# Performance work log

Measured on AMD Instinct MI355X. Metric: run time of the kernel, lower is better.

The kernel has to match this reference:

```python
import jax, jax.numpy as jnp
import numpy as np

N_NODES = 500_000
N_EDGES = 4_000_000


def setup_inputs() -> dict:
    key = jax.random.key(0)
    k1, k2, k3, k4 = jax.random.split(key, 4)
    x = jax.random.normal(k1, (N_NODES, 3), dtype=jnp.float32)
    edge_index = jax.random.randint(k2, (2, N_EDGES), 0, N_NODES, dtype=jnp.int32)
    # GCNConv(3, 16) and GCNConv(16, 1): weight [in, out], bias [out]
    W1 = jax.random.normal(k3, (3, 16), dtype=jnp.float32) / np.sqrt(3.0)
    b1 = jnp.zeros((16,), dtype=jnp.float32)
    W2 = jax.random.normal(k4, (16, 1), dtype=jnp.float32) / np.sqrt(16.0)
    b2 = jnp.zeros((1,), dtype=jnp.float32)
    return {"x": x, "edge_index": edge_index, "W1": W1, "b1": b1, "W2": W2, "b2": b2}


def gcn_conv(x, edge_index, W, b):
    """PyG GCNConv: add self-loops, symmetric deg^-1/2 normalization,
    linear transform, scatter-add aggregation to target nodes, bias."""
    n = x.shape[0]
    loop = jnp.arange(n, dtype=edge_index.dtype)
    row = jnp.concatenate([edge_index[0], loop])  # source nodes
    col = jnp.concatenate([edge_index[1], loop])  # target nodes
    deg = jax.ops.segment_sum(jnp.ones_like(col, dtype=x.dtype), col, num_segments=n)
    deg_inv_sqrt = jnp.where(deg > 0, jax.lax.rsqrt(jnp.maximum(deg, 1.0)), 0.0)
    norm = deg_inv_sqrt[row] * deg_inv_sqrt[col]  # [E+N]
    h = x @ W  # [N, out]
    msg = h[row] * norm[:, None]  # gather + scale, [E+N, out]
    out = jax.ops.segment_sum(msg, col, num_segments=n)  # scatter-add
    return out + b


def reference(x, edge_index, W1, b1, W2, b2):
    h = jax.nn.relu(gcn_conv(x, edge_index, W1, b1))
    return gcn_conv(h, edge_index, W2, b2)  # [N, 1]
```

## Files before the change

### kernel.cpp

```cpp
#include <hip/hip_runtime.h>
#include <hip/hip_fp16.h>


typedef float vf4 __attribute__((ext_vector_type(4)));

#define NB 512
#define SHIFT 10
#define SLICE 1024
#define CAP 11264
#define P1T 1024
#define P1PER 16
#define P1G 256
#define SENT 0xFFFFFFFFu

__global__ __launch_bounds__(1024) void p1_partition(
        const int* __restrict__ row, const int* __restrict__ col,
        unsigned* __restrict__ gcur, unsigned* __restrict__ buf, int E) {
    __shared__ unsigned hist[NB];
    __shared__ unsigned loff[NB], lcur[NB], gbase[NB];
    __shared__ unsigned stage[P1T * P1PER];
    __shared__ unsigned wsum[16];
    int t = threadIdx.x;
    if (t < NB) hist[t] = 0;
    __syncthreads();
    int per = (E + P1G - 1) / P1G;
    per = (per + 3) & ~3;
    long long base = (long long)blockIdx.x * per;
    long long eend = base + per; if (eend > E) eend = E;
    int nch = (per + 4095) / 4096;
    unsigned ent[P1PER];
    int bkt[P1PER];
#pragma unroll
    for (int ch = 0; ch < 4; ch++) {
        if (ch < nch) {
            long long e = base + (long long)ch * 4096 + 4 * t;
            if (e + 3 < eend) {
                int4 c4 = *(const int4*)(col + e);
                int4 r4 = *(const int4*)(row + e);
                int cs[4] = {c4.x, c4.y, c4.z, c4.w};
                int rs[4] = {r4.x, r4.y, r4.z, r4.w};
#pragma unroll
                for (int u = 0; u < 4; u++) {
                    int j = ch * 4 + u;
                    ent[j] = ((unsigned)rs[u] << SHIFT) | (unsigned)(cs[u] & (SLICE - 1));
                    bkt[j] = cs[u] >> SHIFT;
                    atomicAdd(&hist[bkt[j]], 1u);
                }
            } else {
#pragma unroll
                for (int u = 0; u < 4; u++) {
                    int j = ch * 4 + u;
                    long long ee = e + u;
                    if (ee < eend) {
                        int c = col[ee], r = row[ee];
                        ent[j] = ((unsigned)r << SHIFT) | (unsigned)(c & (SLICE - 1));
                        bkt[j] = c >> SHIFT;
                        atomicAdd(&hist[bkt[j]], 1u);
                    } else bkt[j] = -1;
                }
            }
        } else {
#pragma unroll
            for (int u = 0; u < 4; u++) bkt[ch * 4 + u] = -1;
        }
    }
    __syncthreads();
    unsigned myc = 0, v = 0;
    int lane = t & 63, w = t >> 6;
    if (t < NB) {
        myc = hist[t];
        v = myc;
#pragma unroll
        for (int d = 1; d < 64; d <<= 1) {
            unsigned o = __shfl_up(v, d, 64);
            if (lane >= d) v += o;
        }
        if (lane == 63) wsum[w] = v;
    }
    __syncthreads();
    if (w == 0) {
        unsigned s = (lane < 8) ? wsum[lane] : 0u, sv = s;
#pragma unroll
        for (int d = 1; d < 8; d <<= 1) {
            unsigned o = __shfl_up(sv, d, 64);
            if (lane >= d) sv += o;
        }
        if (lane < 8) wsum[lane] = sv - s;
    }
    __syncthreads();
    if (t < NB) {
        unsigned excl = v - myc + wsum[w];
        loff[t] = excl;
        lcur[t] = excl;
        unsigned padded = (myc + 15u) & ~15u;
        gbase[t] = padded ? atomicAdd(&gcur[t], padded) : 0u;
        hist[t] = padded;
    }
    __syncthreads();
#pragma unroll
    for (int j = 0; j < P1PER; j++) {
        if (bkt[j] >= 0) {
            unsigned p = atomicAdd(&lcur[bkt[j]], 1u);
            stage[p] = ent[j];
        }
    }
    __syncthreads();
    if (t < NB) {
        unsigned c = myc, padded = hist[t], lo = loff[t], gb = gbase[t];
        unsigned* dst = buf + (size_t)t * CAP + gb;
        for (unsigned s = 0; s + 4 <= padded && gb + s + 4 <= CAP; s += 4) {
            uint4 q;
            q.x = (s + 0 < c) ? stage[lo + s + 0] : SENT;
            q.y = (s + 1 < c) ? stage[lo + s + 1] : SENT;
            q.z = (s + 2 < c) ? stage[lo + s + 2] : SENT;
            q.w = (s + 3 < c) ? stage[lo + s + 3] : SENT;
            *(uint4*)(dst + s) = q;
        }
    }
}

__global__ __launch_bounds__(1024) void k2a(
        const unsigned* __restrict__ gcur, const unsigned* __restrict__ buf,
        const float* __restrict__ x, float* __restrict__ dis,
        uint2* __restrict__ xs4h, unsigned* __restrict__ pstart,
        unsigned* __restrict__ buf2, int N) {
    __shared__ unsigned sorted[CAP];
    __shared__ unsigned cnts[SLICE];
    __shared__ unsigned pos[SLICE];
    __shared__ unsigned wsum[16];
    __shared__ unsigned stot;
    int b = blockIdx.x, t = threadIdx.x;
    cnts[t] = 0;
    __syncthreads();
    unsigned ext = min(gcur[b], (unsigned)CAP);
    const unsigned* bp = buf + (size_t)b * CAP;
    for (unsigned i = 4 * t; i < ext; i += 4096) {
        uint4 q = *(const uint4*)(bp + i);
        if (q.x != SENT) atomicAdd(&cnts[q.x & (SLICE - 1)], 1u);
        if (q.y != SENT) atomicAdd(&cnts[q.y & (SLICE - 1)], 1u);
        if (q.z != SENT) atomicAdd(&cnts[q.z & (SLICE - 1)], 1u);
        if (q.w != SENT) atomicAdd(&cnts[q.w & (SLICE - 1)], 1u);
    }
    __syncthreads();
    unsigned myc = cnts[t];
    unsigned v = myc;
    int lane = t & 63, w = t >> 6;
#pragma unroll
    for (int d = 1; d < 64; d <<= 1) {
        unsigned o = __shfl_up(v, d, 64);
        if (lane >= d) v += o;
    }
    if (lane == 63) wsum[w] = v;
    __syncthreads();
    if (w == 0) {
        unsigned s = (lane < 16) ? wsum[lane] : 0u, sv = s;
#pragma unroll
        for (int d = 1; d < 16; d <<= 1) {
            unsigned o = __shfl_up(sv, d, 64);
            if (lane >= d) sv += o;
        }
        if (lane < 16) wsum[lane] = sv - s;
    }
    __syncthreads();
    unsigned excl = v - myc + wsum[w];
    pos[t] = excl;
    if (t == 1023) stot = excl + myc;
    int c = (b << SHIFT) + t;
    if (c < N) {
        float d = rsqrtf(1.0f + (float)myc);
        dis[c] = d;
        __half2 h01 = __floats2half2_rn(d * x[3 * c], d * x[3 * c + 1]);
        __half2 h23 = __floats2half2_rn(d * x[3 * c + 2], 0.f);
        uint2 u;
        u.x = *(unsigned*)&h01;
        u.y = *(unsigned*)&h23;
        xs4h[c] = u;
        pstart[c] = (excl << 8) | min(myc, 255u);
    }
    __syncthreads();
    for (unsigned i = 4 * t; i < ext; i += 4096) {
        uint4 q = *(const uint4*)(bp + i);
        if (q.x != SENT) { unsigned p = atomicAdd(&pos[q.x & (SLICE - 1)], 1u); sorted[p] = q.x >> SHIFT; }
        if (q.y != SENT) { unsigned p = atomicAdd(&pos[q.y & (SLICE - 1)], 1u); sorted[p] = q.y >> SHIFT; }
        if (q.z != SENT) { unsigned p = atomicAdd(&pos[q.z & (SLICE - 1)], 1u); sorted[p] = q.z >> SHIFT; }
        if (q.w != SENT) { unsigned p = atomicAdd(&pos[q.w & (SLICE - 1)], 1u); sorted[p] = q.w >> SHIFT; }
    }
    __syncthreads();
    unsigned tot = stot;
    unsigned* b2p = buf2 + (size_t)b * CAP;
    for (unsigned i = t; i < tot; i += 1024) b2p[i] = sorted[i];
}

__global__ __launch_bounds__(1024) void k2b(
        const unsigned* __restrict__ pstart, const unsigned* __restrict__ buf2,
        const uint2* __restrict__ xs4h, const float* __restrict__ dis,
        const float* __restrict__ W1, const float* __restrict__ b1,
        const float* __restrict__ W2, float* __restrict__ hs2, int N) {
    __shared__ float sW[48], sb[16], sw2[16];
    int b = blockIdx.x, t = threadIdx.x;
    if (t < 48) sW[t] = W1[t];
    if (t < 16) { sb[t] = b1[t]; sw2[t] = W2[t]; }
    __syncthreads();
    int c = (b << SHIFT) + t;
    if (c >= N) return;
    unsigned meta = pstart[c];
    const unsigned* sp = buf2 + (size_t)b * CAP + (meta >> 8);
    unsigned cnt = meta & 255u;
    float d = dis[c];
    uint2 us = xs4h[c];
    float2 fs = __half22float2(*(__half2*)&us.x);
    float a0 = fs.x, a1 = fs.y, a2 = __low2float(*(__half2*)&us.y);
    unsigned j = 0;
    for (; j + 4 <= cnt; j += 4) {
        unsigned r0 = sp[j], r1 = sp[j + 1], r2 = sp[j + 2], r3 = sp[j + 3];
        uint2 u0 = xs4h[r0], u1 = xs4h[r1], u2 = xs4h[r2], u3 = xs4h[r3];
        float2 f0 = __half22float2(*(__half2*)&u0.x); float g0 = __low2float(*(__half2*)&u0.y);
        float2 f1 = __half22float2(*(__half2*)&u1.x); float g1 = __low2float(*(__half2*)&u1.y);
        float2 f2 = __half22float2(*(__half2*)&u2.x); float g2 = __low2float(*(__half2*)&u2.y);
        float2 f3 = __half22float2(*(__half2*)&u3.x); float g3 = __low2float(*(__half2*)&u3.y);
        a0 += (f0.x + f1.x) + (f2.x + f3.x);
        a1 += (f0.y + f1.y) + (f2.y + f3.y);
        a2 += (g0 + g1) + (g2 + g3);
    }
    for (; j < cnt; j++) {
        uint2 u = xs4h[sp[j]];
        float2 f = __half22float2(*(__half2*)&u.x);
        a0 += f.x; a1 += f.y; a2 += __low2float(*(__half2*)&u.y);
    }
    float s = 0.f;
#pragma unroll
    for (int k = 0; k < 16; k++) {
        float z = fmaxf(d * (a0 * sW[k] + a1 * sW[16 + k] + a2 * sW[32 + k]) + sb[k], 0.f);
        s += z * sw2[k];
    }
    hs2[c] = d * s;
}

__global__ __launch_bounds__(1024) void k2c(
        const unsigned* __restrict__ pstart, const unsigned* __restrict__ buf2,
        const float* __restrict__ hs2, const float* __restrict__ dis,
        const float* __restrict__ b2, float* __restrict__ out, int N) {
    int b = blockIdx.x, t = threadIdx.x;
    int c = (b << SHIFT) + t;
    if (c >= N) return;
    unsigned meta = pstart[c];
    const unsigned* sp = buf2 + (size_t)b * CAP + (meta >> 8);
    unsigned cnt = meta & 255u;
    float s = hs2[c];
    unsigned j = 0;
    for (; j + 4 <= cnt; j += 4) {
        unsigned r0 = sp[j], r1 = sp[j + 1], r2 = sp[j + 2], r3 = sp[j + 3];
        float v0 = hs2[r0], v1 = hs2[r1], v2 = hs2[r2], v3 = hs2[r3];
        s += (v0 + v1) + (v2 + v3);
    }
    for (; j < cnt; j++) s += hs2[sp[j]];
    out[c] = dis[c] * s + b2[0];
}

__global__ void fb_deg(const int* __restrict__ col, float* __restrict__ deg, int E) {
    int e = blockIdx.x * blockDim.x + threadIdx.x;
    if (e < E) atomicAdd(&deg[col[e]], 1.0f);
}
__global__ void fb_pass_a(const float* __restrict__ x, const float* __restrict__ deg,
                          float* __restrict__ dis, vf4* __restrict__ xs4, int N) {
    int i = blockIdx.x * blockDim.x + threadIdx.x;
    if (i >= N) return;
    float d = rsqrtf(deg[i] + 1.0f);
    dis[i] = d;
    vf4 v; v.x = d * x[3 * i]; v.y = d * x[3 * i + 1]; v.z = d * x[3 * i + 2]; v.w = 0.f;
    xs4[i] = v;
}
__global__ void fb_aggx(const int* __restrict__ ei, const float* __restrict__ xs4,
                        float* __restrict__ accx, int E) {
    int t = blockIdx.x * blockDim.x + threadIdx.x;
    int e = t >> 2, k = t & 3;
    if (e >= E) return;
    int r = ei[e], c = ei[E + e];
    float val = xs4[4 * r + k];
    if (k < 3) atomicAdd(&accx[4 * c + k], val);
}
__global__ void fb_post1(const vf4* __restrict__ accx, const vf4* __restrict__ xs4,
                         const float* __restrict__ dis, const float* __restrict__ W1,
                         const float* __restrict__ b1, const float* __restrict__ W2,
                         float* __restrict__ hs2, int N) {
    __shared__ float sW[48], sb[16], sw2[16];
    if (threadIdx.x < 48) sW[threadIdx.x] = W1[threadIdx.x];
    if (threadIdx.x < 16) { sb[threadIdx.x] = b1[threadIdx.x]; sw2[threadIdx.x] = W2[threadIdx.x]; }
    __syncthreads();
    int i = blockIdx.x * blockDim.x + threadIdx.x;
    if (i >= N) return;
    vf4 a = accx[i], self = xs4[i];
    float a0 = a.x + self.x, a1 = a.y + self.y, a2 = a.z + self.z;
    float d = dis[i], s = 0.f;
#pragma unroll
    for (int k = 0; k < 16; k++) {
        float z = fmaxf(d * (a0 * sW[k] + a1 * sW[16 + k] + a2 * sW[32 + k]) + sb[k], 0.f);
        s += z * sw2[k];
    }
    hs2[i] = d * s;
}
__global__ void fb_agg2(const int* __restrict__ ei, const float* __restrict__ hs2,
                        float* __restrict__ acc2, int E) {
    int e = blockIdx.x * blockDim.x + threadIdx.x;
    if (e >= E) return;
    atomicAdd(&acc2[ei[E + e]], hs2[ei[e]]);
}
__global__ void fb_fin(const float* __restrict__ acc2, const float* __restrict__ hs2,
                       const float* __restrict__ dis, const float* __restrict__ b2,
                       float* __restrict__ out, int N) {
    int i = blockIdx.x * blockDim.x + threadIdx.x;
    if (i < N) out[i] = dis[i] * (acc2[i] + hs2[i]) + b2[0];
}

extern "C" void kernel_launch(void* const* d_in, const int* in_sizes, int n_in,
                              void* d_out, int out_size, void* d_ws, size_t ws_size,
                              hipStream_t stream) {
    const float* x  = (const float*)d_in[0];
    const int*   ei = (const int*)d_in[1];
    const float* W1 = (const float*)d_in[2];
    const float* b1 = (const float*)d_in[3];
    const float* W2 = (const float*)d_in[4];
    const float* b2 = (const float*)d_in[5];
    float* out = (float*)d_out;

    const int N = in_sizes[0] / 3;
    const int E = in_sizes[1] / 2;
    const int* row = ei;
    const int* col = ei + E;

    float* ws = (float*)d_ws;
    size_t need = (size_t)(1024 + 2 * (size_t)NB * CAP + 5 * (size_t)N) * 4;

    if (ws_size >= need) {
        unsigned* gcur = (unsigned*)ws;
        unsigned* buf  = (unsigned*)ws + 1024;
        unsigned* buf2 = buf + (size_t)NB * CAP;
        float* dis  = (float*)(buf2 + (size_t)NB * CAP);
        uint2* xs4h = (uint2*)(dis + N);
        float* hs2  = dis + 3 * (size_t)N;
        unsigned* pstart = (unsigned*)(dis + 4 * (size_t)N);

        hipMemsetAsync(gcur, 0, 1024 * sizeof(unsigned), stream);
        p1_partition<<<P1G, P1T, 0, stream>>>(row, col, gcur, buf, E);
        k2a<<<NB, 1024, 0, stream>>>(gcur, buf, x, dis, xs4h, pstart, buf2, N);
        k2b<<<NB, 1024, 0, stream>>>(pstart, buf2, xs4h, dis, W1, b1, W2, hs2, N);
        k2c<<<NB, 1024, 0, stream>>>(pstart, buf2, hs2, dis, b2, out, N);
    } else {
        float* deg = ws;
        float* dis = ws + (size_t)N;
        vf4*  xs4 = (vf4*)(ws + 2 * (size_t)N);
        float* accx = ws + 6 * (size_t)N;
        float* hs2 = ws + 10 * (size_t)N;
        float* acc2 = ws + 11 * (size_t)N;
        const int B = 256;
        hipMemsetAsync(deg, 0, (size_t)N * sizeof(float), stream);
        hipMemsetAsync(accx, 0, 4 * (size_t)N * sizeof(float), stream);
        hipMemsetAsync(acc2, 0, (size_t)N * sizeof(float), stream);
        fb_deg<<<(E + B - 1) / B, B, 0, stream>>>(col, deg, E);
        fb_pass_a<<<(N + B - 1) / B, B, 0, stream>>>(x, deg, dis, xs4, N);
        long long t4 = (long long)E * 4;
        fb_aggx<<<(int)((t4 + B - 1) / B), B, 0, stream>>>(ei, (const float*)xs4, accx, E);
        fb_post1<<<(N + B - 1) / B, B, 0, stream>>>((const vf4*)accx, xs4, dis, W1, b1, W2, hs2, N);
        fb_agg2<<<(E + B - 1) / B, B, 0, stream>>>(ei, hs2, acc2, E);
        fb_fin<<<(N + B - 1) / B, B, 0, stream>>>(acc2, hs2, dis, b2, out, N);
    }
}
```

Before: 167.9 us.

## Move bucket scatter into layer-1 aggregation kernel and read neighbors from LDS

The per-slice counting sort is split. k2a1 now only counts, computes 4-padded offsets and writes the fp16 scaled features. The scatter into shared memory moves into the layer-1 aggregation kernel, which then reads neighbor indices straight from LDS as uint4 instead of re-reading them from global memory. The dis array is dropped and recomputed from the stored degree, and the neighbor index loads use aligned uint4 vectors. The cost is a second pass over the bucket buffer in k2bf, plus heavy LDS use that may limit occupancy.

```diff
diff --git a/kernel.cpp b/kernel.cpp
--- a/kernel.cpp
+++ b/kernel.cpp
@@ -119,16 +119,12 @@
     }
 }
 
-__global__ __launch_bounds__(1024) void k2a(
+__global__ __launch_bounds__(1024) void k2a1(
         const unsigned* __restrict__ gcur, const unsigned* __restrict__ buf,
-        const float* __restrict__ x, float* __restrict__ dis,
-        uint2* __restrict__ xs4h, unsigned* __restrict__ pstart,
-        unsigned* __restrict__ buf2, int N) {
-    __shared__ unsigned sorted[CAP];
+        const float* __restrict__ x, uint2* __restrict__ xs4h,
+        unsigned* __restrict__ pstart, int N) {
     __shared__ unsigned cnts[SLICE];
-    __shared__ unsigned pos[SLICE];
     __shared__ unsigned wsum[16];
-    __shared__ unsigned stot;
     int b = blockIdx.x, t = threadIdx.x;
     cnts[t] = 0;
     __syncthreads();
@@ -143,7 +139,8 @@
     }
     __syncthreads();
     unsigned myc = cnts[t];
-    unsigned v = myc;
+    unsigned pc = (myc + 3u) & ~3u;
+    unsigned v = pc;
     int lane = t & 63, w = t >> 6;
 #pragma unroll
     for (int d = 1; d < 64; d <<= 1) {
@@ -162,58 +159,66 @@
         if (lane < 16) wsum[lane] = sv - s;
     }
     __syncthreads();
-    unsigned excl = v - myc + wsum[w];
-    pos[t] = excl;
-    if (t == 1023) stot = excl + myc;
+    unsigned excl = v - pc + wsum[w];
     int c = (b << SHIFT) + t;
+    pstart[c] = (excl << 8) | min(myc, 255u);
     if (c < N) {
         float d = rsqrtf(1.0f + (float)myc);
-        dis[c] = d;
         __half2 h01 = __floats2half2_rn(d * x[3 * c], d * x[3 * c + 1]);
         __half2 h23 = __floats2half2_rn(d * x[3 * c + 2], 0.f);
         uint2 u;
         u.x = *(unsigned*)&h01;
         u.y = *(unsigned*)&h23;
         xs4h[c] = u;
-        pstart[c] = (excl << 8) | min(myc, 255u);
-    }
-    __syncthreads();
-    for (unsigned i = 4 * t; i < ext; i += 4096) {
-        uint4 q = *(const uint4*)(bp + i);
-        if (q.x != SENT) { unsigned p = atomicAdd(&pos[q.x & (SLICE - 1)], 1u); sorted[p] = q.x >> SHIFT; }
-        if (q.y != SENT) { unsigned p = atomicAdd(&pos[q.y & (SLICE - 1)], 1u); sorted[p] = q.y >> SHIFT; }
-        if (q.z != SENT) { unsigned p = atomicAdd(&pos[q.z & (SLICE - 1)], 1u); sorted[p] = q.z >> SHIFT; }
-        if (q.w != SENT) { unsigned p = atomicAdd(&pos[q.w & (SLICE - 1)], 1u); sorted[p] = q.w >> SHIFT; }
-    }
-    __syncthreads();
-    unsigned tot = stot;
-    unsigned* b2p = buf2 + (size_t)b * CAP;
-    for (unsigned i = t; i < tot; i += 1024) b2p[i] = sorted[i];
-}
-
-__global__ __launch_bounds__(1024) void k2b(
-        const unsigned* __restrict__ pstart, const unsigned* __restrict__ buf2,
-        const uint2* __restrict__ xs4h, const float* __restrict__ dis,
+    }
+}
+
+__global__ __launch_bounds__(1024) void k2bf(
+        const unsigned* __restrict__ gcur, const unsigned* __restrict__ buf,
+        const unsigned* __restrict__ pstart, const uint2* __restrict__ xs4h,
         const float* __restrict__ W1, const float* __restrict__ b1,
-        const float* __restrict__ W2, float* __restrict__ hs2, int N) {
+        const float* __restrict__ W2, unsigned* __restrict__ buf2,
+        float* __restrict__ hs2, int N) {
+    __shared__ __align__(16) unsigned sorted[CAP];
+    __shared__ unsigned pos[SLICE];
+    __shared__ unsigned stot;
     __shared__ float sW[48], sb[16], sw2[16];
     int b = blockIdx.x, t = threadIdx.x;
     if (t < 48) sW[t] = W1[t];
     if (t < 16) { sb[t] = b1[t]; sw2[t] = W2[t]; }
-    __syncthreads();
+    unsigned meta = pstart[(b << SHIFT) + t];
+    pos[t] = meta >> 8;
+    if (t == SLICE - 1) {
+        unsigned tt = (meta >> 8) + (((meta & 255u) + 3u) & ~3u);
+        stot = min(tt, (unsigned)CAP);
+    }
+    __syncthreads();
+    unsigned ext = min(gcur[b], (unsigned)CAP);
+    const unsigned* bp = buf + (size_t)b * CAP;
+    for (unsigned i = 4 * t; i < ext; i += 4096) {
+        uint4 q = *(const uint4*)(bp + i);
+        if (q.x != SENT) { unsigned p = atomicAdd(&pos[q.x & (SLICE - 1)], 1u); if (p < CAP) sorted[p] = q.x >> SHIFT; }
+        if (q.y != SENT) { unsigned p = atomicAdd(&pos[q.y & (SLICE - 1)], 1u); if (p < CAP) sorted[p] = q.y >> SHIFT; }
+        if (q.z != SENT) { unsigned p = atomicAdd(&pos[q.z & (SLICE - 1)], 1u); if (p < CAP) sorted[p] = q.z >> SHIFT; }
+        if (q.w != SENT) { unsigned p = atomicAdd(&pos[q.w & (SLICE - 1)], 1u); if (p < CAP) sorted[p] = q.w >> SHIFT; }
+    }
+    __syncthreads();
+    unsigned tot = stot;
+    unsigned* b2p = buf2 + (size_t)b * CAP;
+    for (unsigned i = 4 * t; i < tot; i += 4096)
+        *(uint4*)(b2p + i) = *(const uint4*)(sorted + i);
     int c = (b << SHIFT) + t;
     if (c >= N) return;
-    unsigned meta = pstart[c];
-    const unsigned* sp = buf2 + (size_t)b * CAP + (meta >> 8);
     unsigned cnt = meta & 255u;
-    float d = dis[c];
+    unsigned base = meta >> 8;
+    float d = rsqrtf(1.0f + (float)cnt);
     uint2 us = xs4h[c];
     float2 fs = __half22float2(*(__half2*)&us.x);
     float a0 = fs.x, a1 = fs.y, a2 = __low2float(*(__half2*)&us.y);
     unsigned j = 0;
     for (; j + 4 <= cnt; j += 4) {
-        unsigned r0 = sp[j], r1 = sp[j + 1], r2 = sp[j + 2], r3 = sp[j + 3];
-        uint2 u0 = xs4h[r0], u1 = xs4h[r1], u2 = xs4h[r2], u3 = xs4h[r3];
+        uint4 rr = *(const uint4*)(sorted + base + j);
+        uint2 u0 = xs4h[rr.x], u1 = xs4h[rr.y], u2 = xs4h[rr.z], u3 = xs4h[rr.w];
         float2 f0 = __half22float2(*(__half2*)&u0.x); float g0 = __low2float(*(__half2*)&u0.y);
         float2 f1 = __half22float2(*(__half2*)&u1.x); float g1 = __low2float(*(__half2*)&u1.y);
         float2 f2 = __half22float2(*(__half2*)&u2.x); float g2 = __low2float(*(__half2*)&u2.y);
@@ -223,7 +228,7 @@
         a2 += (g0 + g1) + (g2 + g3);
     }
     for (; j < cnt; j++) {
-        uint2 u = xs4h[sp[j]];
+        uint2 u = xs4h[sorted[base + j]];
         float2 f = __half22float2(*(__half2*)&u.x);
         a0 += f.x; a1 += f.y; a2 += __low2float(*(__half2*)&u.y);
     }
@@ -238,23 +243,24 @@
 
 __global__ __launch_bounds__(1024) void k2c(
         const unsigned* __restrict__ pstart, const unsigned* __restrict__ buf2,
-        const float* __restrict__ hs2, const float* __restrict__ dis,
-        const float* __restrict__ b2, float* __restrict__ out, int N) {
+        const float* __restrict__ hs2, const float* __restrict__ b2,
+        float* __restrict__ out, int N) {
     int b = blockIdx.x, t = threadIdx.x;
     int c = (b << SHIFT) + t;
     if (c >= N) return;
     unsigned meta = pstart[c];
     const unsigned* sp = buf2 + (size_t)b * CAP + (meta >> 8);
     unsigned cnt = meta & 255u;
+    float d = rsqrtf(1.0f + (float)cnt);
     float s = hs2[c];
     unsigned j = 0;
     for (; j + 4 <= cnt; j += 4) {
-        unsigned r0 = sp[j], r1 = sp[j + 1], r2 = sp[j + 2], r3 = sp[j + 3];
-        float v0 = hs2[r0], v1 = hs2[r1], v2 = hs2[r2], v3 = hs2[r3];
+        uint4 rr = *(const uint4*)(sp + j);
+        float v0 = hs2[rr.x], v1 = hs2[rr.y], v2 = hs2[rr.z], v3 = hs2[rr.w];
         s += (v0 + v1) + (v2 + v3);
     }
     for (; j < cnt; j++) s += hs2[sp[j]];
-    out[c] = dis[c] * s + b2[0];
+    out[c] = d * s + b2[0];
 }
 
 __global__ void fb_deg(const int* __restrict__ col, float* __restrict__ deg, int E) {
@@ -329,22 +335,22 @@
     const int* col = ei + E;
 
     float* ws = (float*)d_ws;
-    size_t need = (size_t)(1024 + 2 * (size_t)NB * CAP + 5 * (size_t)N) * 4;
+    size_t need = (size_t)(1024 + 2 * (size_t)NB * CAP + 3 * (size_t)N
+                           + (size_t)NB * SLICE) * 4;
 
     if (ws_size >= need) {
         unsigned* gcur = (unsigned*)ws;
         unsigned* buf  = (unsigned*)ws + 1024;
         unsigned* buf2 = buf + (size_t)NB * CAP;
-        float* dis  = (float*)(buf2 + (size_t)NB * CAP);
-        uint2* xs4h = (uint2*)(dis + N);
-        float* hs2  = dis + 3 * (size_t)N;
-        unsigned* pstart = (unsigned*)(dis + 4 * (size_t)N);
+        uint2* xs4h = (uint2*)(buf2 + (size_t)NB * CAP);
+        float* hs2  = (float*)(xs4h + N);
+        unsigned* pstart = (unsigned*)(hs2 + N);
 
         hipMemsetAsync(gcur, 0, 1024 * sizeof(unsigned), stream);
         p1_partition<<<P1G, P1T, 0, stream>>>(row, col, gcur, buf, E);
-        k2a<<<NB, 1024, 0, stream>>>(gcur, buf, x, dis, xs4h, pstart, buf2, N);
-        k2b<<<NB, 1024, 0, stream>>>(pstart, buf2, xs4h, dis, W1, b1, W2, hs2, N);
-        k2c<<<NB, 1024, 0, stream>>>(pstart, buf2, hs2, dis, b2, out, N);
+        k2a1<<<NB, 1024, 0, stream>>>(gcur, buf, x, xs4h, pstart, N);
+        k2bf<<<NB, 1024, 0, stream>>>(gcur, buf, pstart, xs4h, W1, b1, W2, buf2, hs2, N);
+        k2c<<<NB, 1024, 0, stream>>>(pstart, buf2, hs2, b2, out, N);
     } else {
         float* deg = ws;
         float* dis = ws + (size_t)N;
```

Result: faster. 157.4 us (-6.3%).
